# Performance work log

Hardware: AMD Instinct MI355X
Metric: run time of the kernel (lower is better)

Reference implementation:

```python
import jax, jax.numpy as jnp
import numpy as np

B, S, D, H, L = 64, 512, 512, 512, 2


def gru_cell(x, h, Wih, Whh, bih, bhh):
    # PyTorch GRUCell math: gates ordered (r, z, n)
    gi = x @ Wih.T + bih          # [B, 3H]
    gh = h @ Whh.T + bhh          # [B, 3H]
    ir, iz, i_n = jnp.split(gi, 3, axis=-1)
    hr, hz, h_n = jnp.split(gh, 3, axis=-1)
    r = jax.nn.sigmoid(ir + hr)
    z = jax.nn.sigmoid(iz + hz)
    n = jnp.tanh(i_n + r * h_n)
    return (1.0 - z) * n + z * h


def setup_inputs() -> dict:
    key = jax.random.key(0)
    ks = jax.random.split(key, 12)
    s = 0.05
    inp = {
        "input": jax.random.normal(ks[0], (B, S, D), jnp.float32),
        "encoder_h": jax.random.normal(ks[1], (L, B, 2 * H), jnp.float32),
        # stacked per-layer GRUCell params (input_size == hidden_size so layer dims match)
        "Wih_f": jax.random.normal(ks[2], (L, 3 * H, D), jnp.float32) * s,
        "Whh_f": jax.random.normal(ks[3], (L, 3 * H, H), jnp.float32) * s,
        "bih_f": jax.random.normal(ks[4], (L, 3 * H), jnp.float32) * s,
        "bhh_f": jax.random.normal(ks[5], (L, 3 * H), jnp.float32) * s,
        "Wih_b": jax.random.normal(ks[6], (L, 3 * H, D), jnp.float32) * s,
        "Whh_b": jax.random.normal(ks[7], (L, 3 * H, H), jnp.float32) * s,
        "bih_b": jax.random.normal(ks[8], (L, 3 * H), jnp.float32) * s,
        "bhh_b": jax.random.normal(ks[9], (L, 3 * H), jnp.float32) * s,
    }
    return inp


def reference(input, encoder_h, Wih_f, Whh_f, bih_f, bhh_f, Wih_b, Whh_b, bih_b, bhh_b):
    n_layers = Wih_f.shape[0]
    hidden = Whh_f.shape[-1]
    h_f0 = encoder_h[:, :, :hidden]   # [L, B, H]
    h_b0 = encoder_h[:, :, hidden:]   # [L, B, H]
    xs_f = jnp.swapaxes(input, 0, 1)  # [S, B, D]
    xs_b = jnp.flip(xs_f, axis=0)     # reversed sequence

    def step(carry, xt):
        h_f, h_b = carry
        x_f, x_b = xt
        hf_new, hb_new = [], []
        for j in range(n_layers):
            x_f = gru_cell(x_f, h_f[j], Wih_f[j], Whh_f[j], bih_f[j], bhh_f[j])
            x_b = gru_cell(x_b, h_b[j], Wih_b[j], Whh_b[j], bih_b[j], bhh_b[j])
            hf_new.append(x_f)
            hb_new.append(x_b)
        return (jnp.stack(hf_new), jnp.stack(hb_new)), (x_f, x_b)

    (h_f, h_b), (out_f, out_b) = jax.lax.scan(step, (h_f0, h_b0), (xs_f, xs_b))
    out_f = jnp.swapaxes(out_f, 0, 1)                  # [B, S, H]
    out_b = jnp.flip(jnp.swapaxes(out_b, 0, 1), axis=1)  # un-reverse in time
    out = jnp.concatenate([out_f, out_b], axis=-1)      # [B, S, 2H]
    h = jnp.concatenate([h_f, h_b], axis=-1)            # [L, B, 2H]
    return out, h
```

## Files before the change

### kernel.cpp

```cpp
#include <hip/hip_runtime.h>

constexpr int BATCH = 64;
constexpr int SEQ   = 512;
constexpr int DIN   = 512;
constexpr int HID   = 512;
constexpr int LAY   = 2;
constexpr int G3    = 3 * HID;
constexpr int KPAD  = 522;

typedef __attribute__((ext_vector_type(8))) short bf16x8;
typedef __attribute__((ext_vector_type(4))) float f32x4;
typedef unsigned short u16;
typedef unsigned int   u32;
typedef unsigned long long u64;

__device__ __forceinline__ u16 f2bf(float f) {
  union { float f; u32 u; } v; v.f = f;
  return (u16)((v.u + 0x7fffu + ((v.u >> 16) & 1u)) >> 16);
}

__device__ __forceinline__ u64 ld_agent_u64(const u16* p) {
  return __hip_atomic_load((const u64*)p, __ATOMIC_RELAXED, __HIP_MEMORY_SCOPE_AGENT);
}
__device__ __forceinline__ bf16x8 ld_frag_agent(const u16* p) {
  union { u64 q[2]; bf16x8 f; } u;
  u.q[0] = ld_agent_u64(p);
  u.q[1] = ld_agent_u64(p + 4);
  return u.f;
}
__device__ __forceinline__ void st_agent_u16(u16* p, u16 v) {
  __hip_atomic_store(p, v, __ATOMIC_RELAXED, __HIP_MEMORY_SCOPE_AGENT);
}
__device__ __forceinline__ void st_agent_u32(u32* p, u32 v) {
  __hip_atomic_store(p, v, __ATOMIC_RELAXED, __HIP_MEMORY_SCOPE_AGENT);
}

__device__ __forceinline__ void poll_ge(const u32* flags, u32 target) {
  const int idx = threadIdx.x & 31;
  for (;;) {
    u32 v = __hip_atomic_load(flags + idx, __ATOMIC_RELAXED, __HIP_MEMORY_SCOPE_AGENT);
    #pragma unroll
    for (int off = 16; off >= 1; off >>= 1) {
      u32 o = (u32)__shfl_xor((int)v, off, 64);
      v = v < o ? v : o;
    }
    if (v >= target) break;
    __builtin_amdgcn_s_sleep(1);
  }
  __asm__ volatile("" ::: "memory");
}

struct Params {
  const float* input;
  const float* enc_h;
  const float* Wih[2];
  const float* Whh[2];
  const float* bih[2];
  const float* bhh[2];
  float* out;
  u16* xin;
  u16* wih;
  u16* whh;
  u16* out0;
  u16* hbf;
  u32* flags;
};

__global__ __launch_bounds__(256) void convert_kernel(Params p) {
  const int gtid = blockIdx.x * 256 + threadIdx.x;
  const int nthr = gridDim.x * 256;
  for (int i = gtid; i < BATCH * SEQ * DIN; i += nthr) p.xin[i] = f2bf(p.input[i]);
  for (int d = 0; d < 2; ++d) {
    const float* s1 = p.Wih[d];
    u16* d1 = p.wih + (size_t)d * LAY * G3 * DIN;
    for (int i = gtid; i < LAY * G3 * DIN; i += nthr) d1[i] = f2bf(s1[i]);
    const float* s2 = p.Whh[d];
    u16* d2 = p.whh + (size_t)d * LAY * G3 * HID;
    for (int i = gtid; i < LAY * G3 * HID; i += nthr) d2[i] = f2bf(s2[i]);
  }
  if (gtid < LAY * 2 * 32) p.flags[gtid] = 0;
}

__global__ __launch_bounds__(256, 1) void recur_all(Params p) {
  const int wg    = blockIdx.x;
  const int layer = wg >> 6;
  const int cwg   = wg & 63;
  const int dir   = cwg & 1;
  const int slice = cwg >> 1;
  const int j0    = slice * 16;
  const int wave  = threadIdx.x >> 6;
  const int lane  = threadIdx.x & 63;
  const int lq = lane >> 4, ln = lane & 15;
  const int j = j0 + ln;

  __shared__ u16 lwhh[3][16][KPAD];
  {
    const u16* whh = p.whh + ((size_t)dir * LAY + layer) * G3 * HID;
    for (int idx = threadIdx.x; idx < 3 * 16 * 64; idx += 256) {
      const int k8 = idx & 63, row = idx >> 6;
      const int g = row >> 4, jj = row & 15;
      *(bf16x8*)&lwhh[g][jj][k8 * 8] =
          *(const bf16x8*)(whh + (size_t)(g * HID + j0 + jj) * HID + k8 * 8);
    }
  }

  u16* hbL = p.hbf + (size_t)layer * 2 * 2 * BATCH * HID;
  u16* hb[2] = { hbL + (size_t)dir * BATCH * HID,
                 hbL + (size_t)(2 + dir) * BATCH * HID };

  const u16* wih = p.wih + ((size_t)dir * LAY + layer) * G3 * DIN;
  const u16* bri[3];
  #pragma unroll
  for (int g = 0; g < 3; ++g) bri[g] = wih + (size_t)(g * HID + j) * DIN;

  const float* bih = p.bih[dir] + (size_t)layer * G3;
  const float* bhh = p.bhh[dir] + (size_t)layer * G3;
  const float b_r  = bih[j] + bhh[j];
  const float b_z  = bih[HID + j] + bhh[HID + j];
  const float bi_n = bih[2 * HID + j];
  const float bh_n = bhh[2 * HID + j];

  float hreg[4];
  #pragma unroll
  for (int i = 0; i < 4; ++i) {
    const int m = wave * 16 + lq * 4 + i;
    hreg[i] = p.enc_h[((size_t)layer * BATCH + m) * (2 * HID) + (size_t)dir * HID + j];
    st_agent_u16(&hb[0][(size_t)m * HID + j], f2bf(hreg[i]));
  }

  u32* fown  = p.flags + (size_t)(layer * 2 + dir) * 32;
  u32* fdep  = p.flags + (size_t)dir * 32;
  u32* fslot = fown + slice;

  __threadfence_block();
  __syncthreads();
  if (threadIdx.x == 0) st_agent_u32(fslot, 1);

  const int am = wave * 16 + ln;
  float* hsec = p.out + (size_t)BATCH * SEQ * 2 * HID;

  f32x4 accx[3];
  if (layer == 1) poll_ge(fdep, 2);
  accx[0] = f32x4{0, 0, 0, 0}; accx[1] = accx[0]; accx[2] = accx[0];
  if (layer == 0) {
    const u16* ax = p.xin + ((size_t)am * SEQ + (dir ? SEQ - 1 : 0)) * DIN;
    #pragma unroll 4
    for (int k0 = 0; k0 < 512; k0 += 32) {
      const int koff = k0 + lq * 8;
      const bf16x8 a_x = *(const bf16x8*)(ax + koff);
      #pragma unroll
      for (int g = 0; g < 3; ++g)
        accx[g] = __builtin_amdgcn_mfma_f32_16x16x32_bf16(
            a_x, *(const bf16x8*)(bri[g] + koff), accx[g], 0, 0, 0);
    }
  } else {
    const u16* ax = p.out0 + ((size_t)dir * SEQ * BATCH + am) * HID;
    bf16x8 fx[16];
    #pragma unroll
    for (int kk = 0; kk < 16; ++kk) fx[kk] = ld_frag_agent(ax + kk * 32 + lq * 8);
    #pragma unroll
    for (int kk = 0; kk < 16; ++kk) {
      const int koff = kk * 32 + lq * 8;
      #pragma unroll
      for (int g = 0; g < 3; ++g)
        accx[g] = __builtin_amdgcn_mfma_f32_16x16x32_bf16(
            fx[kk], *(const bf16x8*)(bri[g] + koff), accx[g], 0, 0, 0);
    }
  }
  poll_ge(fown, 1);

  for (int t = 0; t < SEQ; ++t) {
    const u16* ah = hb[t & 1] + (size_t)am * HID;
    bf16x8 fh[16];
    #pragma unroll
    for (int kk = 0; kk < 16; ++kk) fh[kk] = ld_frag_agent(ah + kk * 32 + lq * 8);
    f32x4 acch[3];
    acch[0] = f32x4{0, 0, 0, 0}; acch[1] = acch[0]; acch[2] = acch[0];
    #pragma unroll
    for (int kk = 0; kk < 16; ++kk) {
      const int koff = kk * 32 + lq * 8;
      #pragma unroll
      for (int g = 0; g < 3; ++g)
        acch[g] = __builtin_amdgcn_mfma_f32_16x16x32_bf16(
            fh[kk], *(const bf16x8*)&lwhh[g][ln][koff], acch[g], 0, 0, 0);
    }

    u16* hwrite = hb[(t + 1) & 1];
    #pragma unroll
    for (int i = 0; i < 4; ++i) {
      const int m = wave * 16 + lq * 4 + i;
      const float r = 1.f / (1.f + __expf(-(accx[0][i] + acch[0][i] + b_r)));
      const float z = 1.f / (1.f + __expf(-(accx[1][i] + acch[1][i] + b_z)));
      const float n = tanhf(accx[2][i] + bi_n + r * (acch[2][i] + bh_n));
      const float hnew = (1.f - z) * n + z * hreg[i];
      hreg[i] = hnew;
      if (t + 1 < SEQ) st_agent_u16(&hwrite[(size_t)m * HID + j], f2bf(hnew));
      if (layer == 0) {
        st_agent_u16(&p.out0[(((size_t)dir * SEQ + t) * BATCH + m) * HID + j], f2bf(hnew));
      } else {
        const int tt = dir ? (SEQ - 1 - t) : t;
        p.out[((size_t)m * SEQ + tt) * (2 * HID) + (size_t)dir * HID + j] = hnew;
      }
      if (t == SEQ - 1)
        hsec[((size_t)layer * BATCH + m) * (2 * HID) + (size_t)dir * HID + j] = hnew;
    }

    __threadfence_block();
    __syncthreads();
    if (threadIdx.x == 0) st_agent_u32(fslot, (u32)(t + 2));

    if (t + 1 < SEQ) {
      if (layer == 1) poll_ge(fdep, (u32)(t + 3));
      const int tn = t + 1;
      accx[0] = f32x4{0, 0, 0, 0}; accx[1] = accx[0]; accx[2] = accx[0];
      if (layer == 0) {
        const u16* ax = p.xin + ((size_t)am * SEQ + (dir ? SEQ - 1 - tn : tn)) * DIN;
        #pragma unroll 4
        for (int k0 = 0; k0 < 512; k0 += 32) {
          const int koff = k0 + lq * 8;
          const bf16x8 a_x = *(const bf16x8*)(ax + koff);
          #pragma unroll
          for (int g = 0; g < 3; ++g)
            accx[g] = __builtin_amdgcn_mfma_f32_16x16x32_bf16(
                a_x, *(const bf16x8*)(bri[g] + koff), accx[g], 0, 0, 0);
        }
      } else {
        const u16* ax = p.out0 + (((size_t)dir * SEQ + tn) * BATCH + am) * HID;
        bf16x8 fx[16];
        #pragma unroll
        for (int kk = 0; kk < 16; ++kk) fx[kk] = ld_frag_agent(ax + kk * 32 + lq * 8);
        #pragma unroll
        for (int kk = 0; kk < 16; ++kk) {
          const int koff = kk * 32 + lq * 8;
          #pragma unroll
          for (int g = 0; g < 3; ++g)
            accx[g] = __builtin_amdgcn_mfma_f32_16x16x32_bf16(
                fx[kk], *(const bf16x8*)(bri[g] + koff), accx[g], 0, 0, 0);
        }
      }
      poll_ge(fown, (u32)(t + 2));
    }
  }
}

extern "C" void kernel_launch(void* const* d_in, const int* in_sizes, int n_in,
                              void* d_out, int out_size, void* d_ws, size_t ws_size,
                              hipStream_t stream) {
  Params p;
  p.input  = (const float*)d_in[0];
  p.enc_h  = (const float*)d_in[1];
  p.Wih[0] = (const float*)d_in[2];
  p.Whh[0] = (const float*)d_in[3];
  p.bih[0] = (const float*)d_in[4];
  p.bhh[0] = (const float*)d_in[5];
  p.Wih[1] = (const float*)d_in[6];
  p.Whh[1] = (const float*)d_in[7];
  p.bih[1] = (const float*)d_in[8];
  p.bhh[1] = (const float*)d_in[9];
  p.out = (float*)d_out;

  uintptr_t base = (uintptr_t)d_ws;
  size_t off = 0;
  auto take = [&](size_t bytes) -> void* {
    void* r = (void*)(base + off);
    off += (bytes + 255) & ~(size_t)255;
    return r;
  };
  p.xin   = (u16*)take((size_t)BATCH * SEQ * DIN * 2);
  p.wih   = (u16*)take((size_t)2 * LAY * G3 * DIN * 2);
  p.whh   = (u16*)take((size_t)2 * LAY * G3 * HID * 2);
  p.out0  = (u16*)take((size_t)2 * SEQ * BATCH * HID * 2);
  p.hbf   = (u16*)take((size_t)LAY * 2 * 2 * BATCH * HID * 2);
  p.flags = (u32*)take((size_t)LAY * 2 * 32 * 4);
  if (off > ws_size) return;

  convert_kernel<<<dim3(2048), dim3(256), 0, stream>>>(p);
  recur_all<<<dim3(128), dim3(256), 0, stream>>>(p);
}
```

Measured before the change: 8.405 ms.

## Split layer paths, use per-step out0 slots as layer-0 hidden state, stage layer-1 h in LDS

Result: faster. 6.875 ms (-18.2%).

```diff
diff --git a/kernel.cpp b/kernel.cpp
--- a/kernel.cpp
+++ b/kernel.cpp
@@ -7,6 +7,8 @@
 constexpr int LAY   = 2;
 constexpr int G3    = 3 * HID;
 constexpr int KPAD  = 522;
+constexpr int SLOTS = SEQ + 1;
+constexpr int HPAD  = 520;
 
 typedef __attribute__((ext_vector_type(8))) short bf16x8;
 typedef __attribute__((ext_vector_type(4))) float f32x4;
@@ -21,12 +23,6 @@
 
 __device__ __forceinline__ u64 ld_agent_u64(const u16* p) {
   return __hip_atomic_load((const u64*)p, __ATOMIC_RELAXED, __HIP_MEMORY_SCOPE_AGENT);
-}
-__device__ __forceinline__ bf16x8 ld_frag_agent(const u16* p) {
-  union { u64 q[2]; bf16x8 f; } u;
-  u.q[0] = ld_agent_u64(p);
-  u.q[1] = ld_agent_u64(p + 4);
-  return u.f;
 }
 __device__ __forceinline__ void st_agent_u16(u16* p, u16 v) {
   __hip_atomic_store(p, v, __ATOMIC_RELAXED, __HIP_MEMORY_SCOPE_AGENT);
@@ -45,6 +41,18 @@
       v = v < o ? v : o;
     }
     if (v >= target) break;
+    __builtin_amdgcn_s_sleep(1);
+  }
+  __asm__ volatile("" ::: "memory");
+}
+
+__device__ __forceinline__ void poll_both(const u32* flags, int dir, u32 tdep, u32 town) {
+  const int l = threadIdx.x & 63;
+  const u32* addr = flags + (size_t)dir * 32 + (l & 31) + ((l >> 5) * 64);
+  const u32 tgt = (l < 32) ? tdep : town;
+  for (;;) {
+    u32 v = __hip_atomic_load(addr, __ATOMIC_RELAXED, __HIP_MEMORY_SCOPE_AGENT);
+    if (__all((int)(v >= tgt))) break;
     __builtin_amdgcn_s_sleep(1);
   }
   __asm__ volatile("" ::: "memory");
@@ -94,6 +102,8 @@
   const int j = j0 + ln;
 
   __shared__ u16 lwhh[3][16][KPAD];
+  __shared__ u16 hstage[BATCH][HPAD];
+
   {
     const u16* whh = p.whh + ((size_t)dir * LAY + layer) * G3 * HID;
     for (int idx = threadIdx.x; idx < 3 * 16 * 64; idx += 256) {
@@ -104,9 +114,9 @@
     }
   }
 
-  u16* hbL = p.hbf + (size_t)layer * 2 * 2 * BATCH * HID;
-  u16* hb[2] = { hbL + (size_t)dir * BATCH * HID,
-                 hbL + (size_t)(2 + dir) * BATCH * HID };
+  u16* o0 = p.out0 + (size_t)dir * SLOTS * BATCH * HID;
+  u16* hb[2] = { p.hbf + (size_t)dir * BATCH * HID,
+                 p.hbf + (size_t)(2 + dir) * BATCH * HID };
 
   const u16* wih = p.wih + ((size_t)dir * LAY + layer) * G3 * DIN;
   const u16* bri[3];
@@ -125,12 +135,13 @@
   for (int i = 0; i < 4; ++i) {
     const int m = wave * 16 + lq * 4 + i;
     hreg[i] = p.enc_h[((size_t)layer * BATCH + m) * (2 * HID) + (size_t)dir * HID + j];
-    st_agent_u16(&hb[0][(size_t)m * HID + j], f2bf(hreg[i]));
+    if (layer == 0) st_agent_u16(&o0[(size_t)m * HID + j], f2bf(hreg[i]));
+    else            st_agent_u16(&hb[0][(size_t)m * HID + j], f2bf(hreg[i]));
   }
 
   u32* fown  = p.flags + (size_t)(layer * 2 + dir) * 32;
+  u32* fslot = fown + slice;
   u32* fdep  = p.flags + (size_t)dir * 32;
-  u32* fslot = fown + slice;
 
   __threadfence_block();
   __syncthreads();
@@ -139,82 +150,59 @@
   const int am = wave * 16 + ln;
   float* hsec = p.out + (size_t)BATCH * SEQ * 2 * HID;
 
-  f32x4 accx[3];
-  if (layer == 1) poll_ge(fdep, 2);
-  accx[0] = f32x4{0, 0, 0, 0}; accx[1] = accx[0]; accx[2] = accx[0];
   if (layer == 0) {
-    const u16* ax = p.xin + ((size_t)am * SEQ + (dir ? SEQ - 1 : 0)) * DIN;
-    #pragma unroll 4
-    for (int k0 = 0; k0 < 512; k0 += 32) {
-      const int koff = k0 + lq * 8;
-      const bf16x8 a_x = *(const bf16x8*)(ax + koff);
-      #pragma unroll
-      for (int g = 0; g < 3; ++g)
-        accx[g] = __builtin_amdgcn_mfma_f32_16x16x32_bf16(
-            a_x, *(const bf16x8*)(bri[g] + koff), accx[g], 0, 0, 0);
-    }
-  } else {
-    const u16* ax = p.out0 + ((size_t)dir * SEQ * BATCH + am) * HID;
-    bf16x8 fx[16];
-    #pragma unroll
-    for (int kk = 0; kk < 16; ++kk) fx[kk] = ld_frag_agent(ax + kk * 32 + lq * 8);
-    #pragma unroll
-    for (int kk = 0; kk < 16; ++kk) {
-      const int koff = kk * 32 + lq * 8;
-      #pragma unroll
-      for (int g = 0; g < 3; ++g)
-        accx[g] = __builtin_amdgcn_mfma_f32_16x16x32_bf16(
-            fx[kk], *(const bf16x8*)(bri[g] + koff), accx[g], 0, 0, 0);
-    }
-  }
-  poll_ge(fown, 1);
-
-  for (int t = 0; t < SEQ; ++t) {
-    const u16* ah = hb[t & 1] + (size_t)am * HID;
-    bf16x8 fh[16];
-    #pragma unroll
-    for (int kk = 0; kk < 16; ++kk) fh[kk] = ld_frag_agent(ah + kk * 32 + lq * 8);
-    f32x4 acch[3];
-    acch[0] = f32x4{0, 0, 0, 0}; acch[1] = acch[0]; acch[2] = acch[0];
-    #pragma unroll
-    for (int kk = 0; kk < 16; ++kk) {
-      const int koff = kk * 32 + lq * 8;
-      #pragma unroll
-      for (int g = 0; g < 3; ++g)
-        acch[g] = __builtin_amdgcn_mfma_f32_16x16x32_bf16(
-            fh[kk], *(const bf16x8*)&lwhh[g][ln][koff], acch[g], 0, 0, 0);
-    }
-
-    u16* hwrite = hb[(t + 1) & 1];
-    #pragma unroll
-    for (int i = 0; i < 4; ++i) {
-      const int m = wave * 16 + lq * 4 + i;
-      const float r = 1.f / (1.f + __expf(-(accx[0][i] + acch[0][i] + b_r)));
-      const float z = 1.f / (1.f + __expf(-(accx[1][i] + acch[1][i] + b_z)));
-      const float n = tanhf(accx[2][i] + bi_n + r * (acch[2][i] + bh_n));
-      const float hnew = (1.f - z) * n + z * hreg[i];
-      hreg[i] = hnew;
-      if (t + 1 < SEQ) st_agent_u16(&hwrite[(size_t)m * HID + j], f2bf(hnew));
-      if (layer == 0) {
-        st_agent_u16(&p.out0[(((size_t)dir * SEQ + t) * BATCH + m) * HID + j], f2bf(hnew));
-      } else {
-        const int tt = dir ? (SEQ - 1 - t) : t;
-        p.out[((size_t)m * SEQ + tt) * (2 * HID) + (size_t)dir * HID + j] = hnew;
-      }
-      if (t == SEQ - 1)
-        hsec[((size_t)layer * BATCH + m) * (2 * HID) + (size_t)dir * HID + j] = hnew;
-    }
-
-    __threadfence_block();
-    __syncthreads();
-    if (threadIdx.x == 0) st_agent_u32(fslot, (u32)(t + 2));
-
-    if (t + 1 < SEQ) {
-      if (layer == 1) poll_ge(fdep, (u32)(t + 3));
-      const int tn = t + 1;
-      accx[0] = f32x4{0, 0, 0, 0}; accx[1] = accx[0]; accx[2] = accx[0];
-      if (layer == 0) {
+    f32x4 accx[3];
+    accx[0] = f32x4{0, 0, 0, 0}; accx[1] = accx[0]; accx[2] = accx[0];
+    {
+      const u16* ax = p.xin + ((size_t)am * SEQ + (dir ? SEQ - 1 : 0)) * DIN;
+      #pragma unroll 4
+      for (int k0 = 0; k0 < 512; k0 += 32) {
+        const int koff = k0 + lq * 8;
+        const bf16x8 a_x = *(const bf16x8*)(ax + koff);
+        #pragma unroll
+        for (int g = 0; g < 3; ++g)
+          accx[g] = __builtin_amdgcn_mfma_f32_16x16x32_bf16(
+              a_x, *(const bf16x8*)(bri[g] + koff), accx[g], 0, 0, 0);
+      }
+    }
+    poll_ge(fown, 1);
+
+    for (int t = 0; t < SEQ; ++t) {
+      const u16* ah = o0 + (size_t)t * BATCH * HID + (size_t)am * HID;
+      f32x4 acch[3];
+      acch[0] = f32x4{0, 0, 0, 0}; acch[1] = acch[0]; acch[2] = acch[0];
+      #pragma unroll 4
+      for (int k0 = 0; k0 < 512; k0 += 32) {
+        const int koff = k0 + lq * 8;
+        const bf16x8 a_h = *(const bf16x8*)(ah + koff);
+        #pragma unroll
+        for (int g = 0; g < 3; ++g)
+          acch[g] = __builtin_amdgcn_mfma_f32_16x16x32_bf16(
+              a_h, *(const bf16x8*)&lwhh[g][ln][koff], acch[g], 0, 0, 0);
+      }
+
+      u16* ow = o0 + (size_t)(t + 1) * BATCH * HID;
+      #pragma unroll
+      for (int i = 0; i < 4; ++i) {
+        const int m = wave * 16 + lq * 4 + i;
+        const float r = 1.f / (1.f + __expf(-(accx[0][i] + acch[0][i] + b_r)));
+        const float z = 1.f / (1.f + __expf(-(accx[1][i] + acch[1][i] + b_z)));
+        const float n = tanhf(accx[2][i] + bi_n + r * (acch[2][i] + bh_n));
+        const float hnew = (1.f - z) * n + z * hreg[i];
+        hreg[i] = hnew;
+        st_agent_u16(&ow[(size_t)m * HID + j], f2bf(hnew));
+        if (t == SEQ - 1)
+          hsec[(size_t)m * (2 * HID) + (size_t)dir * HID + j] = hnew;
+      }
+
+      __threadfence_block();
+      __syncthreads();
+      if (threadIdx.x == 0) st_agent_u32(fslot, (u32)(t + 2));
+
+      if (t + 1 < SEQ) {
+        const int tn = t + 1;
         const u16* ax = p.xin + ((size_t)am * SEQ + (dir ? SEQ - 1 - tn : tn)) * DIN;
+        accx[0] = f32x4{0, 0, 0, 0}; accx[1] = accx[0]; accx[2] = accx[0];
         #pragma unroll 4
         for (int k0 = 0; k0 < 512; k0 += 32) {
           const int koff = k0 + lq * 8;
@@ -224,21 +212,111 @@
             accx[g] = __builtin_amdgcn_mfma_f32_16x16x32_bf16(
                 a_x, *(const bf16x8*)(bri[g] + koff), accx[g], 0, 0, 0);
         }
-      } else {
-        const u16* ax = p.out0 + (((size_t)dir * SEQ + tn) * BATCH + am) * HID;
-        bf16x8 fx[16];
-        #pragma unroll
-        for (int kk = 0; kk < 16; ++kk) fx[kk] = ld_frag_agent(ax + kk * 32 + lq * 8);
-        #pragma unroll
-        for (int kk = 0; kk < 16; ++kk) {
-          const int koff = kk * 32 + lq * 8;
+        poll_ge(fown, (u32)(t + 2));
+      }
+    }
+  } else {
+    f32x4 accx[3];
+    accx[0] = f32x4{0, 0, 0, 0}; accx[1] = accx[0]; accx[2] = accx[0];
+    poll_ge(fdep, 2);
+    {
+      const u16* ax = o0 + (size_t)1 * BATCH * HID + (size_t)am * HID;
+      #pragma unroll 4
+      for (int k0 = 0; k0 < 512; k0 += 32) {
+        const int koff = k0 + lq * 8;
+        const bf16x8 a_x = *(const bf16x8*)(ax + koff);
+        #pragma unroll
+        for (int g = 0; g < 3; ++g)
+          accx[g] = __builtin_amdgcn_mfma_f32_16x16x32_bf16(
+              a_x, *(const bf16x8*)(bri[g] + koff), accx[g], 0, 0, 0);
+      }
+    }
+    poll_ge(fown, 1);
+
+    {
+      const u16* src = hb[0];
+      u64 q0[16], q1[16];
+      #pragma unroll
+      for (int it = 0; it < 16; ++it) {
+        const u16* sp = src + ((size_t)(it * 256) + threadIdx.x) * 8;
+        q0[it] = ld_agent_u64(sp);
+        q1[it] = ld_agent_u64(sp + 4);
+      }
+      #pragma unroll
+      for (int it = 0; it < 16; ++it) {
+        const int flat = it * 256 + threadIdx.x;
+        u64* dp = (u64*)&hstage[flat >> 6][(flat & 63) * 8];
+        dp[0] = q0[it]; dp[1] = q1[it];
+      }
+    }
+
+    for (int t = 0; t < SEQ; ++t) {
+      __syncthreads();
+
+      f32x4 acch[3];
+      acch[0] = f32x4{0, 0, 0, 0}; acch[1] = acch[0]; acch[2] = acch[0];
+      #pragma unroll
+      for (int kk = 0; kk < 16; ++kk) {
+        const int koff = kk * 32 + lq * 8;
+        const bf16x8 a_h = *(const bf16x8*)&hstage[am][koff];
+        #pragma unroll
+        for (int g = 0; g < 3; ++g)
+          acch[g] = __builtin_amdgcn_mfma_f32_16x16x32_bf16(
+              a_h, *(const bf16x8*)&lwhh[g][ln][koff], acch[g], 0, 0, 0);
+      }
+
+      u16* hwrite = hb[(t + 1) & 1];
+      const int tt = dir ? (SEQ - 1 - t) : t;
+      #pragma unroll
+      for (int i = 0; i < 4; ++i) {
+        const int m = wave * 16 + lq * 4 + i;
+        const float r = 1.f / (1.f + __expf(-(accx[0][i] + acch[0][i] + b_r)));
+        const float z = 1.f / (1.f + __expf(-(accx[1][i] + acch[1][i] + b_z)));
+        const float n = tanhf(accx[2][i] + bi_n + r * (acch[2][i] + bh_n));
+        const float hnew = (1.f - z) * n + z * hreg[i];
+        hreg[i] = hnew;
+        if (t + 1 < SEQ) st_agent_u16(&hwrite[(size_t)m * HID + j], f2bf(hnew));
+        p.out[((size_t)m * SEQ + tt) * (2 * HID) + (size_t)dir * HID + j] = hnew;
+        if (t == SEQ - 1)
+          hsec[((size_t)BATCH + m) * (2 * HID) + (size_t)dir * HID + j] = hnew;
+      }
+
+      __threadfence_block();
+      __syncthreads();
+      if (threadIdx.x == 0) st_agent_u32(fslot, (u32)(t + 2));
+
+      if (t + 1 < SEQ) {
+        const int tn = t + 1;
+        poll_both(p.flags, dir, (u32)(tn + 2), (u32)(t + 2));
+
+        const u16* src = hb[(t + 1) & 1];
+        u64 q0[16], q1[16];
+        #pragma unroll
+        for (int it = 0; it < 16; ++it) {
+          const u16* sp = src + ((size_t)(it * 256) + threadIdx.x) * 8;
+          q0[it] = ld_agent_u64(sp);
+          q1[it] = ld_agent_u64(sp + 4);
+        }
+
+        const u16* ax = o0 + (size_t)(tn + 1) * BATCH * HID + (size_t)am * HID;
+        accx[0] = f32x4{0, 0, 0, 0}; accx[1] = accx[0]; accx[2] = accx[0];
+        #pragma unroll 4
+        for (int k0 = 0; k0 < 512; k0 += 32) {
+          const int koff = k0 + lq * 8;
+          const bf16x8 a_x = *(const bf16x8*)(ax + koff);
           #pragma unroll
           for (int g = 0; g < 3; ++g)
             accx[g] = __builtin_amdgcn_mfma_f32_16x16x32_bf16(
-                fx[kk], *(const bf16x8*)(bri[g] + koff), accx[g], 0, 0, 0);
+                a_x, *(const bf16x8*)(bri[g] + koff), accx[g], 0, 0, 0);
         }
-      }
-      poll_ge(fown, (u32)(t + 2));
+
+        #pragma unroll
+        for (int it = 0; it < 16; ++it) {
+          const int flat = it * 256 + threadIdx.x;
+          u64* dp = (u64*)&hstage[flat >> 6][(flat & 63) * 8];
+          dp[0] = q0[it]; dp[1] = q1[it];
+        }
+      }
     }
   }
 }
@@ -269,8 +347,8 @@
   p.xin   = (u16*)take((size_t)BATCH * SEQ * DIN * 2);
   p.wih   = (u16*)take((size_t)2 * LAY * G3 * DIN * 2);
   p.whh   = (u16*)take((size_t)2 * LAY * G3 * HID * 2);
-  p.out0  = (u16*)take((size_t)2 * SEQ * BATCH * HID * 2);
-  p.hbf   = (u16*)take((size_t)LAY * 2 * 2 * BATCH * HID * 2);
+  p.out0  = (u16*)take((size_t)2 * SLOTS * BATCH * HID * 2);
+  p.hbf   = (u16*)take((size_t)2 * 2 * BATCH * HID * 2);
   p.flags = (u32*)take((size_t)LAY * 2 * 32 * 4);
   if (off > ws_size) return;
 
```
